# Performance work log

Measured on AMD Instinct MI355X. Metric: run time of the kernel, lower is better.

## Reference

```python
import jax, jax.numpy as jnp
import numpy as np

N_AGENTS = 10
N_ENEMIES = 11
N_ALLIES = 9
H = 64           # rnn_hidden_dim
HYP = 64         # api_hyper_dim
DEPTH = 2        # residual_depth
OWN = 32
EF = 10          # enemy_feats_dim
AF = 10          # ally_feats_dim
N_ACTIONS = 17
BS = 1024


def _hypernet(x, win, bin_, wres, bres, wout, bout):
    # Linear -> ReLU -> DEPTH x (ReLU(Linear)+identity) -> Linear
    h = jax.nn.relu(x @ win + bin_)
    for d in range(DEPTH):
        h = jax.nn.relu(h @ wres[d] + bres[d]) + h
    return h @ wout + bout


def _gru_cell(x, h, wi, wh, bi, bh):
    gi = x @ wi + bi
    gh = h @ wh + bh
    ir, iz, in_ = jnp.split(gi, 3, axis=-1)
    hr, hz, hn = jnp.split(gh, 3, axis=-1)
    r = jax.nn.sigmoid(ir + hr)
    z = jax.nn.sigmoid(iz + hz)
    n = jnp.tanh(in_ + r * hn)
    return (1.0 - z) * n + z * h


def setup_inputs() -> dict:
    key = jax.random.key(0)
    ks = iter(jax.random.split(key, 48))
    def p(shape, s=0.1):
        return jax.random.normal(next(ks), shape, jnp.float32) * s
    N = BS * N_AGENTS
    inp = {
        'own_feats':    p((N, OWN), 1.0),
        'enemy_feats':  p((N * N_ENEMIES, EF), 1.0),
        'ally_feats':   p((N * N_ALLIES, AF), 1.0),
        'hidden_state': p((N, H), 1.0),
        'fc1_w': p((OWN, H)), 'fc1_b': p((H,)),
        'agent_emb': p((N_AGENTS, H)), 'action_emb': p((N_ACTIONS, H)),
        'hen_win': p((EF, HYP)), 'hen_bin': p((HYP,)),
        'hen_wres': p((DEPTH, HYP, HYP)), 'hen_bres': p((DEPTH, HYP)),
        'hen_wout': p((HYP, EF * H)), 'hen_bout': p((EF * H,)),
        'hal_win': p((AF, HYP)), 'hal_bin': p((HYP,)),
        'hal_wres': p((DEPTH, HYP, HYP)), 'hal_bres': p((DEPTH, HYP)),
        'hal_wout': p((HYP, AF * H)), 'hal_bout': p((AF * H,)),
        'gru_wi': p((H, 3 * H)), 'gru_wh': p((H, 3 * H)),
        'gru_bi': p((3 * H,)), 'gru_bh': p((3 * H,)),
        'fc2_w': p((H, 6)), 'fc2_b': p((6,)),
        'how_win': p((EF, HYP)), 'how_bin': p((HYP,)),
        'how_wres': p((DEPTH, HYP, HYP)), 'how_bres': p((DEPTH, HYP)),
        'how_wout': p((HYP, H)), 'how_bout': p((H,)),
        'hob_win': p((EF, HYP)), 'hob_bin': p((HYP,)),
        'hob_wres': p((DEPTH, HYP, HYP)), 'hob_bres': p((DEPTH, HYP)),
        'hob_wout': p((HYP, 1)), 'hob_bout': p((1,)),
        'agent_idx': jax.random.randint(next(ks), (N,), 0, N_AGENTS),
        'last_action_idx': jax.random.randint(next(ks), (N,), 0, N_ACTIONS),
        'bs': BS,
    }
    return inp


def reference(own_feats, enemy_feats, ally_feats, hidden_state,
              fc1_w, fc1_b, agent_emb, action_emb,
              hen_win, hen_bin, hen_wres, hen_bres, hen_wout, hen_bout,
              hal_win, hal_bin, hal_wres, hal_bres, hal_wout, hal_bout,
              gru_wi, gru_wh, gru_bi, gru_bh,
              fc2_w, fc2_b,
              how_win, how_bin, how_wres, how_bres, how_wout, how_bout,
              hob_win, hob_bin, hob_wres, hob_bres, hob_wout, hob_bout,
              agent_idx, last_action_idx, bs):
    N = bs * N_AGENTS
    # own embedding + id embeddings
    emb = own_feats @ fc1_w + fc1_b
    emb = emb + agent_emb[agent_idx] + action_emb[last_action_idx]
    # per-enemy hypernet weights [N*NE, EF, H]; bmm + sum-pool over enemies
    w_en = _hypernet(enemy_feats, hen_win, hen_bin, hen_wres, hen_bres,
                     hen_wout, hen_bout).reshape(-1, EF, H)
    emb_en = jnp.einsum('nf,nfh->nh', enemy_feats, w_en)
    emb_en = emb_en.reshape(N, N_ENEMIES, H).sum(axis=1)
    # per-ally hypernet weights + bmm + sum-pool
    w_al = _hypernet(ally_feats, hal_win, hal_bin, hal_wres, hal_bres,
                     hal_wout, hal_bout).reshape(-1, AF, H)
    emb_al = jnp.einsum('nf,nfh->nh', ally_feats, w_al)
    emb_al = emb_al.reshape(N, N_ALLIES, H).sum(axis=1)
    x = jax.nn.relu(emb + emb_en + emb_al)
    hh = _gru_cell(x, hidden_state.reshape(-1, H), gru_wi, gru_wh, gru_bi, gru_bh)
    q_normal = (hh @ fc2_w + fc2_b).reshape(bs, N_AGENTS, 6)
    # attack-action head: hypernet-generated per-enemy weights/biases
    ow = _hypernet(enemy_feats, how_win, how_bin, how_wres, how_bres,
                   how_wout, how_bout).reshape(N, N_ENEMIES, H)
    ob = _hypernet(enemy_feats, hob_win, hob_bin, hob_wres, hob_bres,
                   hob_wout, hob_bout).reshape(N, N_ENEMIES)
    q_attack = (jnp.einsum('nh,neh->ne', hh, ow) + ob).reshape(bs, N_AGENTS, N_ENEMIES)
    q = jnp.concatenate([q_normal, q_attack], axis=-1)
    return q, hh.reshape(bs, N_AGENTS, H)
```

## Files before the change

### kernel.cpp

```cpp
#include <hip/hip_runtime.h>

#define DI static __device__ __forceinline__

typedef short s16x8 __attribute__((ext_vector_type(8)));
typedef float f32x4 __attribute__((ext_vector_type(4)));
typedef float f32x2 __attribute__((ext_vector_type(2)));
typedef unsigned u32x2 __attribute__((ext_vector_type(2)));

DI unsigned short f2b(float f) {
  union { float f; unsigned u; } v; v.f = f;
  return (unsigned short)((v.u + 0x7FFF + ((v.u >> 16) & 1)) >> 16);
}
DI float b2f(unsigned short s) {
  union { unsigned u; float f; } v; v.u = ((unsigned)s) << 16;
  return v.f;
}
DI unsigned cvtpk(float lo, float hi) {
  unsigned r;
  asm("v_cvt_pk_bf16_f32 %0, %1, %2" : "=v"(r) : "v"(lo), "v"(hi));
  return r;
}
DI f32x4 MFMA(s16x8 a, s16x8 b, f32x4 c) {
  return __builtin_amdgcn_mfma_f32_16x16x32_bf16(a, b, c, 0, 0, 0);
}
DI s16x8 ldg8(const unsigned short* p) { return *(const s16x8*)p; }

#define OFF_WEN   0
#define OFF_WAL   10240
#define OFF_WHOW  20480
#define OFF_WHOB  30720
#define OFF_BGEN  40960
#define OFF_BGAL  83968
#define OFF_WIT   126976
#define OFF_WHT   139264
#define OFF_FC1T  151552
#define OFF_FC2E  153600
#define OFF_HOWT  154624
#define OFF_HOBT  158720
#define SH_END    159744
#define B_EMB_EN  (SH_END*2)
#define B_EMB_AL  (B_EMB_EN + 2621440)
#define B_HB      (B_EMB_AL + 2621440)
#define B_GBF     (B_HB + 40960)

#define XSTR 40
#define HSTR 72
#define PSTR 680

__global__ __launch_bounds__(256) void kprep(
    const float* __restrict__ hen_win, const float* __restrict__ hen_wres,
    const float* __restrict__ hal_win, const float* __restrict__ hal_wres,
    const float* __restrict__ how_win, const float* __restrict__ how_wres,
    const float* __restrict__ hob_win, const float* __restrict__ hob_wres,
    const float* __restrict__ hen_wout, const float* __restrict__ hen_bout,
    const float* __restrict__ hal_wout, const float* __restrict__ hal_bout,
    const float* __restrict__ gru_wi, const float* __restrict__ gru_wh,
    const float* __restrict__ fc1_w, const float* __restrict__ fc2_w,
    const float* __restrict__ how_bout, const float* __restrict__ how_wout,
    const float* __restrict__ hob_wout,
    unsigned short* __restrict__ ws)
{
  const int gid = blockIdx.x * 256 + threadIdx.x;
  const int gsz = gridDim.x * 256;
  for (int i = gid; i < 4 * 10240; i += gsz) {
    int s = i / 10240, idx = i - s * 10240;
    const float* win  = (s == 0) ? hen_win  : (s == 1) ? hal_win  : (s == 2) ? how_win  : hob_win;
    const float* wres = (s == 0) ? hen_wres : (s == 1) ? hal_wres : (s == 2) ? how_wres : hob_wres;
    float v;
    if (idx < 2048) { int n = idx >> 5, k = idx & 31; v = (k < 10) ? win[k*64 + n] : 0.f; }
    else { int r = idx - 2048; int d = r >> 12; int r2 = r & 4095; int n = r2 >> 6, k = r2 & 63;
           v = wres[d*4096 + k*64 + n]; }
    ws[s * 10240 + idx] = f2b(v);
  }
  for (int i = gid; i < 2 * 43008; i += gsz) {
    int s = i / 43008, idx = i - s * 43008;
    const float* wout = s ? hal_wout : hen_wout;
    const float* bout = s ? hal_bout : hen_bout;
    int kl = idx & 31, n = (idx >> 5) & 63, c = idx >> 11;
    int kfg = c * 32 + kl;
    float v = 0.f;
    if (kfg < 640)      { int k = kfg / 10, f = kfg - k * 10; v = wout[k*640 + f*64 + n]; }
    else if (kfg < 650) { v = bout[(kfg - 640)*64 + n]; }
    ws[(s ? OFF_BGAL : OFF_BGEN) + idx] = f2b(v);
  }
  for (int i = gid; i < 2 * 12288; i += gsz) {
    int s = i / 12288, idx = i - s * 12288;
    int n = idx >> 6, k = idx & 63;
    const float* w = s ? gru_wh : gru_wi;
    ws[(s ? OFF_WHT : OFF_WIT) + idx] = f2b(w[k*192 + n]);
  }
  for (int i = gid; i < 2048; i += gsz) { int n = i >> 5, k = i & 31; ws[OFF_FC1T + i] = f2b(fc1_w[k*64 + n]); }
  for (int i = gid; i < 1024; i += gsz) {
    int n = i >> 6, k = i & 63;
    float v = 0.f; if (n < 6) v = fc2_w[k*6 + n]; else if (n == 6) v = how_bout[k];
    ws[OFF_FC2E + i] = f2b(v);
  }
  for (int i = gid; i < 4096; i += gsz) ws[OFF_HOWT + i] = f2b(how_wout[i]);
}

template<int TMAX, bool WLAST>
DI void stack_batch(const unsigned short* __restrict__ x_lds,
                    unsigned short* const (&hbp)[TMAX], const int (&tis)[TMAX], int E,
                    const unsigned short* __restrict__ wg,
                    const float* __restrict__ bin, const float* __restrict__ bres,
                    f32x4 (&hval)[TMAX][4])
{
  const int l = threadIdx.x & 63;
  const int lrow = l & 15, gq = l >> 4, lk8 = gq * 8;
  {
    s16x8 wf[4]; f32x4 bv[4];
#pragma unroll
    for (int mt = 0; mt < 4; mt++) {
      wf[mt] = ldg8(wg + (mt*16 + lrow)*32 + lk8);
      bv[mt] = *(const f32x4*)(bin + mt*16 + gq*4);
    }
#pragma unroll
    for (int tt = 0; tt < TMAX; tt++) {
      if (tis[tt] < E) {
        s16x8 xf = *(const s16x8*)&x_lds[(tis[tt]*16 + lrow)*XSTR + lk8];
#pragma unroll
        for (int mt = 0; mt < 4; mt++) {
          f32x4 d = MFMA(wf[mt], xf, f32x4{0.f,0.f,0.f,0.f});
#pragma unroll
          for (int r = 0; r < 4; r++) hval[tt][mt][r] = fmaxf(d[r] + bv[mt][r], 0.f);
        }
        unsigned short* wr = hbp[tt] + lrow*HSTR;
#pragma unroll
        for (int mt = 0; mt < 4; mt++) {
          u32x2 pw;
          pw.x = cvtpk(hval[tt][mt][0], hval[tt][mt][1]);
          pw.y = cvtpk(hval[tt][mt][2], hval[tt][mt][3]);
          *(u32x2*)&wr[mt*16 + gq*4] = pw;
        }
      }
    }
  }
#pragma unroll
  for (int d = 0; d < 2; d++) {
    const unsigned short* wt = wg + 2048 + d * 4096;
    s16x8 wf[4][2]; f32x4 bv[4];
#pragma unroll
    for (int mt = 0; mt < 4; mt++) {
      wf[mt][0] = ldg8(wt + (mt*16 + lrow)*64 + lk8);
      wf[mt][1] = ldg8(wt + (mt*16 + lrow)*64 + 32 + lk8);
      bv[mt] = *(const f32x4*)(bres + d*64 + mt*16 + gq*4);
    }
#pragma unroll
    for (int tt = 0; tt < TMAX; tt++) {
      if (tis[tt] < E) {
        const unsigned short* hr = hbp[tt] + lrow*HSTR;
        s16x8 b0 = *(const s16x8*)&hr[lk8];
        s16x8 b1 = *(const s16x8*)&hr[32 + lk8];
#pragma unroll
        for (int mt = 0; mt < 4; mt++) {
          f32x4 a = MFMA(wf[mt][0], b0, f32x4{0.f,0.f,0.f,0.f});
          a = MFMA(wf[mt][1], b1, a);
#pragma unroll
          for (int r = 0; r < 4; r++)
            hval[tt][mt][r] = fmaxf(a[r] + bv[mt][r], 0.f) + hval[tt][mt][r];
        }
        if (d == 0 || WLAST) {
          unsigned short* wr = hbp[tt] + lrow*HSTR;
#pragma unroll
          for (int mt = 0; mt < 4; mt++) {
            u32x2 pw;
            pw.x = cvtpk(hval[tt][mt][0], hval[tt][mt][1]);
            pw.y = cvtpk(hval[tt][mt][2], hval[tt][mt][3]);
            *(u32x2*)&wr[mt*16 + gq*4] = pw;
          }
        }
      }
    }
  }
}

template<int E>
DI void hyp_body16(const float* __restrict__ feats,
                   const unsigned short* __restrict__ Wg, const unsigned short* __restrict__ Bg,
                   const float* __restrict__ bin, const float* __restrict__ bres,
                   float* __restrict__ emb, char* smem)
{
  unsigned short* x_lds = (unsigned short*)smem;
  unsigned short* h_lds = (unsigned short*)(smem + 14080);
  unsigned short* P     = (unsigned short*)smem;
  const int t = threadIdx.x;
  const int l = t & 63, wv = t >> 6;
  const int lrow = l & 15, gq = l >> 4, lk8 = gq * 8, lr4 = gq * 4;

  for (int idx = t; idx < E * 512; idx += 256) {
    int row = idx >> 5, c = idx & 31;
    x_lds[row*XSTR + c] = (c < 10) ? f2b(feats[row*10 + c]) : (unsigned short)0;
  }
  __syncthreads();

  int tis[3] = {wv, wv + 4, wv + 8};
  unsigned short* hbp[3] = { h_lds + (wv)*16*HSTR, h_lds + (wv+4)*16*HSTR, h_lds + (wv+8)*16*HSTR };
  f32x4 hval[3][4];
  stack_batch<3, true>(x_lds, hbp, tis, E, Wg, bin, bres, hval);
  __syncthreads();

  const int a = t >> 4, kq = t & 15, k0 = kq * 4;
  float acc[4][10];
#pragma unroll
  for (int kk = 0; kk < 4; kk++)
#pragma unroll
    for (int f = 0; f < 10; f++) acc[kk][f] = 0.f;
#pragma unroll
  for (int e = 0; e < E; e++) {
    int row = a * E + e;
    const unsigned short* xr = x_lds + row * XSTR;
    s16x8 xv8 = *(const s16x8*)xr;
    unsigned xv2 = *(const unsigned*)(xr + 8);
    float xf[10];
#pragma unroll
    for (int f = 0; f < 8; f++) xf[f] = b2f((unsigned short)xv8[f]);
    xf[8] = b2f((unsigned short)(xv2 & 0xFFFF));
    xf[9] = b2f((unsigned short)(xv2 >> 16));
    u32x2 hp = *(const u32x2*)&h_lds[row*HSTR + k0];
    float hf[4] = { b2f((unsigned short)(hp.x & 0xFFFF)), b2f((unsigned short)(hp.x >> 16)),
                    b2f((unsigned short)(hp.y & 0xFFFF)), b2f((unsigned short)(hp.y >> 16)) };
#pragma unroll
    for (int kk = 0; kk < 4; kk++)
#pragma unroll
      for (int f = 0; f < 10; f++) acc[kk][f] += hf[kk] * xf[f];
  }
  float sxv = 0.f; int a2 = 0, fx = 0;
  if (t < 160) {
    a2 = t / 10; fx = t - a2 * 10;
    for (int e = 0; e < E; e++) sxv += feats[(a2*E + e)*10 + fx];
  }
  __syncthreads();

  u32x2* Pw = (u32x2*)(P + a*PSTR + k0*10);
#pragma unroll
  for (int m = 0; m < 10; m++) {
    const int s0 = 4*m, s1 = 4*m+1, s2 = 4*m+2, s3 = 4*m+3;
    u32x2 pw;
    pw.x = cvtpk(acc[s0/10][s0%10], acc[s1/10][s1%10]);
    pw.y = cvtpk(acc[s2/10][s2%10], acc[s3/10][s3%10]);
    Pw[m] = pw;
  }
  if (t < 160) P[a2*PSTR + 640 + fx] = f2b(sxv);
  for (int i = t; i < 352; i += 256) { int a3 = i / 22, c = i - a3*22; P[a3*PSTR + 650 + c] = 0; }
  __syncthreads();

  f32x4 acc0 = {0.f,0.f,0.f,0.f}, acc1 = {0.f,0.f,0.f,0.f};
  const unsigned short* Bw = Bg + (wv*16 + lrow)*32 + lk8;
#pragma unroll
  for (int c = 0; c < 21; c++) {
    s16x8 af = *(const s16x8*)&P[lrow*PSTR + c*32 + lk8];
    s16x8 bf = ldg8(Bw + c*2048);
    if (c & 1) acc1 = MFMA(af, bf, acc1); else acc0 = MFMA(af, bf, acc0);
  }
#pragma unroll
  for (int r = 0; r < 4; r++)
    emb[(lr4 + r)*64 + wv*16 + lrow] = acc0[r] + acc1[r];
}

__global__ __launch_bounds__(256) void khyp_ea(
    const float* __restrict__ en_feats, const float* __restrict__ al_feats,
    const unsigned short* __restrict__ ws,
    const float* __restrict__ en_bin, const float* __restrict__ en_bres,
    const float* __restrict__ al_bin, const float* __restrict__ al_bres,
    float* __restrict__ emb_en, float* __restrict__ emb_al)
{
  __shared__ __align__(16) char smem[39424];
  if (blockIdx.x < 640) {
    int blk = blockIdx.x;
    hyp_body16<11>(en_feats + (long)blk*1760, ws + OFF_WEN, ws + OFF_BGEN,
                   en_bin, en_bres, emb_en + (long)blk*1024, smem);
  } else {
    int blk = blockIdx.x - 640;
    hyp_body16<9>(al_feats + (long)blk*1440, ws + OFF_WAL, ws + OFF_BGAL,
                  al_bin, al_bres, emb_al + (long)blk*1024, smem);
  }
}

__global__ __launch_bounds__(256) void kfused(
    const float* __restrict__ own, const float* __restrict__ agent_emb,
    const float* __restrict__ action_emb,
    const int* __restrict__ agent_idx, const int* __restrict__ last_action,
    const float* __restrict__ emb_en, const float* __restrict__ emb_al,
    const float* __restrict__ hidden,
    const unsigned short* __restrict__ ws,
    const float* __restrict__ fc1_b, const float* __restrict__ bi,
    const float* __restrict__ bh, const float* __restrict__ fc2_b,
    float* __restrict__ qout, float* __restrict__ hhout,
    unsigned short* __restrict__ g_bf, float* __restrict__ hb)
{
  __shared__ unsigned short own_lds[16*32];
  __shared__ unsigned short x_lds[16*HSTR];
  __shared__ unsigned short hp_lds[16*HSTR];
  __shared__ unsigned short hh_lds[16*HSTR];
  const int t = threadIdx.x;
  const int l = t & 63, wv = t >> 6;
  const int lrow = l & 15, lk8 = (l >> 4) * 8, lr4 = (l >> 4) * 4;
  const int n0 = blockIdx.x * 16;

  const unsigned short* fc1T = ws + OFF_FC1T;
  const unsigned short* wiT  = ws + OFF_WIT;
  const unsigned short* whT  = ws + OFF_WHT;
  const unsigned short* howT = ws + OFF_HOWT;
  const unsigned short* fc2e = ws + OFF_FC2E;

  for (int i = t; i < 512; i += 256) own_lds[i] = f2b(own[n0*32 + i]);
  for (int i = t; i < 1024; i += 256) hp_lds[(i >> 6)*HSTR + (i & 63)] = f2b(hidden[n0*64 + i]);
  __syncthreads();

  const int j = wv * 16 + lrow;
  {
    s16x8 a0 = *(const s16x8*)&own_lds[lrow*32 + lk8];
    s16x8 b0 = ldg8(fc1T + (wv*16 + lrow)*32 + lk8);
    f32x4 c0 = MFMA(a0, b0, f32x4{0.f,0.f,0.f,0.f});
    float fb = fc1_b[j];
#pragma unroll
    for (int r = 0; r < 4; r++) {
      int aa = lr4 + r; int n = n0 + aa;
      int ai = agent_idx[n], la = last_action[n];
      float v = c0[r] + fb + agent_emb[ai*64 + j] + action_emb[la*64 + j]
              + emb_en[n*64 + j] + emb_al[n*64 + j];
      x_lds[aa*HSTR + j] = f2b(fmaxf(v, 0.f));
    }
  }
  __syncthreads();

  {
    s16x8 xa[2], ha[2];
#pragma unroll
    for (int s = 0; s < 2; s++) {
      xa[s] = *(const s16x8*)&x_lds[lrow*HSTR + s*32 + lk8];
      ha[s] = *(const s16x8*)&hp_lds[lrow*HSTR + s*32 + lk8];
    }
    f32x4 gi[3], gh[3];
#pragma unroll
    for (int g3 = 0; g3 < 3; g3++) { gi[g3] = f32x4{0.f,0.f,0.f,0.f}; gh[g3] = f32x4{0.f,0.f,0.f,0.f}; }
#pragma unroll
    for (int g3 = 0; g3 < 3; g3++) {
      int tl = wv + g3 * 4;
#pragma unroll
      for (int s = 0; s < 2; s++) {
        gi[g3] = MFMA(xa[s], ldg8(wiT + (tl*16 + lrow)*64 + s*32 + lk8), gi[g3]);
        gh[g3] = MFMA(ha[s], ldg8(whT + (tl*16 + lrow)*64 + s*32 + lk8), gh[g3]);
      }
    }
    float bir = bi[j], biz = bi[64 + j], bin_ = bi[128 + j];
    float bhr = bh[j], bhz = bh[64 + j], bhn = bh[128 + j];
#pragma unroll
    for (int r = 0; r < 4; r++) {
      int aa = lr4 + r; int n = n0 + aa;
      float rr = 1.f / (1.f + __expf(-(gi[0][r] + bir + gh[0][r] + bhr)));
      float zz = 1.f / (1.f + __expf(-(gi[1][r] + biz + gh[1][r] + bhz)));
      float nn = tanhf(gi[2][r] + bin_ + rr * (gh[2][r] + bhn));
      float hp = hidden[n*64 + j];
      float hhv = (1.f - zz) * nn + zz * hp;
      hhout[n*64 + j] = hhv;
      hh_lds[aa*HSTR + j] = f2b(hhv);
    }
  }
  __syncthreads();

  {
    s16x8 hha[2];
#pragma unroll
    for (int s = 0; s < 2; s++) hha[s] = *(const s16x8*)&hh_lds[lrow*HSTR + s*32 + lk8];
    f32x4 gc = {0.f,0.f,0.f,0.f};
#pragma unroll
    for (int s = 0; s < 2; s++) gc = MFMA(hha[s], ldg8(howT + (wv*16 + lrow)*64 + s*32 + lk8), gc);
#pragma unroll
    for (int r = 0; r < 4; r++) g_bf[(n0 + lr4 + r)*64 + wv*16 + lrow] = f2b(gc[r]);
    if (wv == 0) {
      f32x4 qc = {0.f,0.f,0.f,0.f};
#pragma unroll
      for (int s = 0; s < 2; s++) qc = MFMA(hha[s], ldg8(fc2e + lrow*64 + s*32 + lk8), qc);
#pragma unroll
      for (int r = 0; r < 4; r++) {
        int n = n0 + lr4 + r;
        if (lrow < 6)       qout[n*17 + lrow] = qc[r] + fc2_b[lrow];
        else if (lrow == 6) hb[n] = qc[r];
      }
    }
  }
}

__global__ __launch_bounds__(256) void kattack(
    const float* __restrict__ en_feats, const unsigned short* __restrict__ ws,
    const float* __restrict__ how_bin, const float* __restrict__ how_bres,
    const float* __restrict__ hob_bin, const float* __restrict__ hob_bres,
    const unsigned short* __restrict__ g_bf, const float* __restrict__ hbuf,
    const float* __restrict__ hob_wout, const float* __restrict__ hob_bout,
    float* __restrict__ qout)
{
  __shared__ __align__(16) char smem[41728];
  unsigned short* x_lds = (unsigned short*)smem;
  unsigned short* scr   = (unsigned short*)(smem + 14080);
  const int t = threadIdx.x;
  const int l = t & 63, wv = t >> 6;
  const int lrow = l & 15, gq = l >> 4;
  const int blk = blockIdx.x;
  const float* feats = en_feats + (long)blk * 1760;

  for (int idx = t; idx < 176*32; idx += 256) {
    int row = idx >> 5, c = idx & 31;
    x_lds[row*XSTR + c] = (c < 10) ? f2b(feats[row*10 + c]) : (unsigned short)0;
  }
  __syncthreads();

  int tis[3] = {wv, wv + 4, wv + 8};
  unsigned short* hbp[3] = { scr + (wv*3+0)*16*HSTR, scr + (wv*3+1)*16*HSTR, scr + (wv*3+2)*16*HSTR };
  f32x4 hval[3][4];

  stack_batch<3, false>(x_lds, hbp, tis, 11, ws + OFF_WHOB, hob_bin, hob_bres, hval);
  f32x4 hw[4];
#pragma unroll
  for (int mt = 0; mt < 4; mt++) hw[mt] = *(const f32x4*)(hob_wout + mt*16 + gq*4);
  float qbv[3] = {0.f, 0.f, 0.f};
#pragma unroll
  for (int tt = 0; tt < 3; tt++) {
    if (tis[tt] < 11) {
      float s = 0.f;
#pragma unroll
      for (int mt = 0; mt < 4; mt++)
#pragma unroll
        for (int r = 0; r < 4; r++) s += hval[tt][mt][r] * hw[mt][r];
      s += __shfl_xor(s, 16, 64);
      s += __shfl_xor(s, 32, 64);
      qbv[tt] = s;
    }
  }

  stack_batch<3, false>(x_lds, hbp, tis, 11, ws + OFF_WHOW, how_bin, how_bres, hval);
  const float hob_b0 = hob_bout[0];
#pragma unroll
  for (int tt = 0; tt < 3; tt++) {
    if (tis[tt] < 11) {
      int row = tis[tt]*16 + lrow;
      int ag = (unsigned)row / 11u;
      int n = blk*16 + ag;
      float s = 0.f;
#pragma unroll
      for (int mt = 0; mt < 4; mt++) {
        u32x2 gv = *(const u32x2*)(g_bf + (long)n*64 + mt*16 + gq*4);
        s += hval[tt][mt][0] * b2f((unsigned short)(gv.x & 0xFFFF))
           + hval[tt][mt][1] * b2f((unsigned short)(gv.x >> 16))
           + hval[tt][mt][2] * b2f((unsigned short)(gv.y & 0xFFFF))
           + hval[tt][mt][3] * b2f((unsigned short)(gv.y >> 16));
      }
      s += __shfl_xor(s, 16, 64);
      s += __shfl_xor(s, 32, 64);
      if (l < 16) {
        int e = row - ag * 11;
        qout[n*17 + 6 + e] = s + qbv[tt] + hbuf[n] + hob_b0;
      }
    }
  }
}

extern "C" void kernel_launch(void* const* d_in, const int* in_sizes, int n_in,
                              void* d_out, int out_size, void* d_ws, size_t ws_size,
                              hipStream_t stream)
{
  (void)in_sizes; (void)n_in; (void)out_size; (void)ws_size;
  const float* own        = (const float*)d_in[0];
  const float* enemy      = (const float*)d_in[1];
  const float* ally       = (const float*)d_in[2];
  const float* hidden     = (const float*)d_in[3];
  const float* fc1_w      = (const float*)d_in[4];
  const float* fc1_b      = (const float*)d_in[5];
  const float* agent_emb  = (const float*)d_in[6];
  const float* action_emb = (const float*)d_in[7];
  const float* hen_win  = (const float*)d_in[8];  const float* hen_bin  = (const float*)d_in[9];
  const float* hen_wres = (const float*)d_in[10]; const float* hen_bres = (const float*)d_in[11];
  const float* hen_wout = (const float*)d_in[12]; const float* hen_bout = (const float*)d_in[13];
  const float* hal_win  = (const float*)d_in[14]; const float* hal_bin  = (const float*)d_in[15];
  const float* hal_wres = (const float*)d_in[16]; const float* hal_bres = (const float*)d_in[17];
  const float* hal_wout = (const float*)d_in[18]; const float* hal_bout = (const float*)d_in[19];
  const float* gru_wi = (const float*)d_in[20];   const float* gru_wh = (const float*)d_in[21];
  const float* gru_bi = (const float*)d_in[22];   const float* gru_bh = (const float*)d_in[23];
  const float* fc2_w  = (const float*)d_in[24];   const float* fc2_b  = (const float*)d_in[25];
  const float* how_win  = (const float*)d_in[26]; const float* how_bin  = (const float*)d_in[27];
  const float* how_wres = (const float*)d_in[28]; const float* how_bres = (const float*)d_in[29];
  const float* how_wout = (const float*)d_in[30]; const float* how_bout = (const float*)d_in[31];
  const float* hob_win  = (const float*)d_in[32]; const float* hob_bin  = (const float*)d_in[33];
  const float* hob_wres = (const float*)d_in[34]; const float* hob_bres = (const float*)d_in[35];
  const float* hob_wout = (const float*)d_in[36]; const float* hob_bout = (const float*)d_in[37];
  const int* agent_idx   = (const int*)d_in[38];
  const int* last_action = (const int*)d_in[39];

  unsigned short* ws = (unsigned short*)d_ws;
  float* emb_en = (float*)((char*)d_ws + B_EMB_EN);
  float* emb_al = (float*)((char*)d_ws + B_EMB_AL);
  float* hb     = (float*)((char*)d_ws + B_HB);
  unsigned short* g_bf = (unsigned short*)((char*)d_ws + B_GBF);

  float* q  = (float*)d_out;
  float* hh = q + 1024*10*17;

  kprep<<<128, 256, 0, stream>>>(hen_win, hen_wres, hal_win, hal_wres,
      how_win, how_wres, hob_win, hob_wres,
      hen_wout, hen_bout, hal_wout, hal_bout,
      gru_wi, gru_wh, fc1_w, fc2_w, how_bout, how_wout, hob_wout, ws);
  khyp_ea<<<1280, 256, 0, stream>>>(enemy, ally, ws,
      hen_bin, hen_bres, hal_bin, hal_bres, emb_en, emb_al);
  kfused<<<640, 256, 0, stream>>>(own, agent_emb, action_emb, agent_idx, last_action,
      emb_en, emb_al, hidden, ws, fc1_b, gru_bi, gru_bh, fc2_b, q, hh, g_bf, hb);
  kattack<<<640, 256, 0, stream>>>(enemy, ws, how_bin, how_bres, hob_bin, hob_bres,
      g_bf, hb, hob_wout, hob_bout, q);
}
```

Before: 78.49 us.

## Make hypernet embedding kernel persistent with double-buffered feature staging and swizzled LDS

New measurement: 78.05 us. No clear change (-0.6%).

```diff
diff --git a/kernel.cpp b/kernel.cpp
--- a/kernel.cpp
+++ b/kernel.cpp
@@ -4,7 +4,6 @@
 
 typedef short s16x8 __attribute__((ext_vector_type(8)));
 typedef float f32x4 __attribute__((ext_vector_type(4)));
-typedef float f32x2 __attribute__((ext_vector_type(2)));
 typedef unsigned u32x2 __attribute__((ext_vector_type(2)));
 
 DI unsigned short f2b(float f) {
@@ -36,16 +35,20 @@
 #define OFF_FC1T  151552
 #define OFF_FC2E  153600
 #define OFF_HOWT  154624
-#define OFF_HOBT  158720
 #define SH_END    159744
 #define B_EMB_EN  (SH_END*2)
 #define B_EMB_AL  (B_EMB_EN + 2621440)
 #define B_HB      (B_EMB_AL + 2621440)
 #define B_GBF     (B_HB + 40960)
 
+#define PSTR 680
+#define HSTR 72
 #define XSTR 40
-#define HSTR 72
-#define PSTR 680
+
+#define SLOT 28160
+#define XBC  5632
+DI int xoffc(int row, int b) { return ((row*32  + b) ^ ((row & 7) << 4)); }
+DI int hoffc(int row, int b) { return XBC + ((row*128 + b) ^ ((row & 7) << 4)); }
 
 __global__ __launch_bounds__(256) void kprep(
     const float* __restrict__ hen_win, const float* __restrict__ hen_wres,
@@ -57,7 +60,6 @@
     const float* __restrict__ gru_wi, const float* __restrict__ gru_wh,
     const float* __restrict__ fc1_w, const float* __restrict__ fc2_w,
     const float* __restrict__ how_bout, const float* __restrict__ how_wout,
-    const float* __restrict__ hob_wout,
     unsigned short* __restrict__ ws)
 {
   const int gid = blockIdx.x * 256 + threadIdx.x;
@@ -98,15 +100,21 @@
   for (int i = gid; i < 4096; i += gsz) ws[OFF_HOWT + i] = f2b(how_wout[i]);
 }
 
-template<int TMAX, bool WLAST>
-DI void stack_batch(const unsigned short* __restrict__ x_lds,
-                    unsigned short* const (&hbp)[TMAX], const int (&tis)[TMAX], int E,
-                    const unsigned short* __restrict__ wg,
-                    const float* __restrict__ bin, const float* __restrict__ bres,
-                    f32x4 (&hval)[TMAX][4])
-{
-  const int l = threadIdx.x & 63;
+DI void stage_item(const float* __restrict__ feats, int vrows, char* sl) {
+  for (int idx = threadIdx.x; idx < 176*16; idx += 256) {
+    int row = idx >> 4, c = idx & 15;
+    float v = (row < vrows && c < 10) ? feats[row*10 + c] : 0.f;
+    *(unsigned short*)(sl + xoffc(row, c*2)) = f2b(v);
+  }
+}
+
+DI void stackP(char* sl, int ntiles, const unsigned short* __restrict__ wg,
+               const float* __restrict__ bin, const float* __restrict__ bres)
+{
+  const int l = threadIdx.x & 63, wv = threadIdx.x >> 6;
   const int lrow = l & 15, gq = l >> 4, lk8 = gq * 8;
+  const int tis[3] = {wv, wv + 4, wv + 8};
+  f32x4 hval[3][4];
   {
     s16x8 wf[4]; f32x4 bv[4];
 #pragma unroll
@@ -115,22 +123,18 @@
       bv[mt] = *(const f32x4*)(bin + mt*16 + gq*4);
     }
 #pragma unroll
-    for (int tt = 0; tt < TMAX; tt++) {
-      if (tis[tt] < E) {
-        s16x8 xf = *(const s16x8*)&x_lds[(tis[tt]*16 + lrow)*XSTR + lk8];
+    for (int tt = 0; tt < 3; tt++) {
+      if (tis[tt] < ntiles) {
+        int row = tis[tt]*16 + lrow;
+        s16x8 xf = *(const s16x8*)(sl + xoffc(row, gq*16));
 #pragma unroll
         for (int mt = 0; mt < 4; mt++) {
-          f32x4 d = MFMA(wf[mt], xf, f32x4{0.f,0.f,0.f,0.f});
-#pragma unroll
-          for (int r = 0; r < 4; r++) hval[tt][mt][r] = fmaxf(d[r] + bv[mt][r], 0.f);
-        }
-        unsigned short* wr = hbp[tt] + lrow*HSTR;
-#pragma unroll
-        for (int mt = 0; mt < 4; mt++) {
-          u32x2 pw;
-          pw.x = cvtpk(hval[tt][mt][0], hval[tt][mt][1]);
+          f32x4 d = MFMA(wf[mt], xf, bv[mt]);
+#pragma unroll
+          for (int r = 0; r < 4; r++) hval[tt][mt][r] = fmaxf(d[r], 0.f);
+          u32x2 pw; pw.x = cvtpk(hval[tt][mt][0], hval[tt][mt][1]);
           pw.y = cvtpk(hval[tt][mt][2], hval[tt][mt][3]);
-          *(u32x2*)&wr[mt*16 + gq*4] = pw;
+          *(u32x2*)(sl + hoffc(row, (mt*16 + gq*4)*2)) = pw;
         }
       }
     }
@@ -138,123 +142,33 @@
 #pragma unroll
   for (int d = 0; d < 2; d++) {
     const unsigned short* wt = wg + 2048 + d * 4096;
-    s16x8 wf[4][2]; f32x4 bv[4];
+    s16x8 wf0[4], wf1[4]; f32x4 bv[4];
 #pragma unroll
     for (int mt = 0; mt < 4; mt++) {
-      wf[mt][0] = ldg8(wt + (mt*16 + lrow)*64 + lk8);
-      wf[mt][1] = ldg8(wt + (mt*16 + lrow)*64 + 32 + lk8);
+      wf0[mt] = ldg8(wt + (mt*16 + lrow)*64 + lk8);
+      wf1[mt] = ldg8(wt + (mt*16 + lrow)*64 + 32 + lk8);
       bv[mt] = *(const f32x4*)(bres + d*64 + mt*16 + gq*4);
     }
 #pragma unroll
-    for (int tt = 0; tt < TMAX; tt++) {
-      if (tis[tt] < E) {
-        const unsigned short* hr = hbp[tt] + lrow*HSTR;
-        s16x8 b0 = *(const s16x8*)&hr[lk8];
-        s16x8 b1 = *(const s16x8*)&hr[32 + lk8];
+    for (int tt = 0; tt < 3; tt++) {
+      if (tis[tt] < ntiles) {
+        int row = tis[tt]*16 + lrow;
+        s16x8 b0 = *(const s16x8*)(sl + hoffc(row, gq*16));
+        s16x8 b1 = *(const s16x8*)(sl + hoffc(row, 64 + gq*16));
 #pragma unroll
         for (int mt = 0; mt < 4; mt++) {
-          f32x4 a = MFMA(wf[mt][0], b0, f32x4{0.f,0.f,0.f,0.f});
-          a = MFMA(wf[mt][1], b1, a);
+          f32x4 acc = MFMA(wf0[mt], b0, bv[mt]);
+          acc = MFMA(wf1[mt], b1, acc);
 #pragma unroll
           for (int r = 0; r < 4; r++)
-            hval[tt][mt][r] = fmaxf(a[r] + bv[mt][r], 0.f) + hval[tt][mt][r];
+            hval[tt][mt][r] = fmaxf(acc[r], 0.f) + hval[tt][mt][r];
+          u32x2 pw; pw.x = cvtpk(hval[tt][mt][0], hval[tt][mt][1]);
+          pw.y = cvtpk(hval[tt][mt][2], hval[tt][mt][3]);
+          *(u32x2*)(sl + hoffc(row, (mt*16 + gq*4)*2)) = pw;
         }
-        if (d == 0 || WLAST) {
-          unsigned short* wr = hbp[tt] + lrow*HSTR;
-#pragma unroll
-          for (int mt = 0; mt < 4; mt++) {
-            u32x2 pw;
-            pw.x = cvtpk(hval[tt][mt][0], hval[tt][mt][1]);
-            pw.y = cvtpk(hval[tt][mt][2], hval[tt][mt][3]);
-            *(u32x2*)&wr[mt*16 + gq*4] = pw;
-          }
-        }
-      }
-    }
-  }
-}
-
-template<int E>
-DI void hyp_body16(const float* __restrict__ feats,
-                   const unsigned short* __restrict__ Wg, const unsigned short* __restrict__ Bg,
-                   const float* __restrict__ bin, const float* __restrict__ bres,
-                   float* __restrict__ emb, char* smem)
-{
-  unsigned short* x_lds = (unsigned short*)smem;
-  unsigned short* h_lds = (unsigned short*)(smem + 14080);
-  unsigned short* P     = (unsigned short*)smem;
-  const int t = threadIdx.x;
-  const int l = t & 63, wv = t >> 6;
-  const int lrow = l & 15, gq = l >> 4, lk8 = gq * 8, lr4 = gq * 4;
-
-  for (int idx = t; idx < E * 512; idx += 256) {
-    int row = idx >> 5, c = idx & 31;
-    x_lds[row*XSTR + c] = (c < 10) ? f2b(feats[row*10 + c]) : (unsigned short)0;
-  }
-  __syncthreads();
-
-  int tis[3] = {wv, wv + 4, wv + 8};
-  unsigned short* hbp[3] = { h_lds + (wv)*16*HSTR, h_lds + (wv+4)*16*HSTR, h_lds + (wv+8)*16*HSTR };
-  f32x4 hval[3][4];
-  stack_batch<3, true>(x_lds, hbp, tis, E, Wg, bin, bres, hval);
-  __syncthreads();
-
-  const int a = t >> 4, kq = t & 15, k0 = kq * 4;
-  float acc[4][10];
-#pragma unroll
-  for (int kk = 0; kk < 4; kk++)
-#pragma unroll
-    for (int f = 0; f < 10; f++) acc[kk][f] = 0.f;
-#pragma unroll
-  for (int e = 0; e < E; e++) {
-    int row = a * E + e;
-    const unsigned short* xr = x_lds + row * XSTR;
-    s16x8 xv8 = *(const s16x8*)xr;
-    unsigned xv2 = *(const unsigned*)(xr + 8);
-    float xf[10];
-#pragma unroll
-    for (int f = 0; f < 8; f++) xf[f] = b2f((unsigned short)xv8[f]);
-    xf[8] = b2f((unsigned short)(xv2 & 0xFFFF));
-    xf[9] = b2f((unsigned short)(xv2 >> 16));
-    u32x2 hp = *(const u32x2*)&h_lds[row*HSTR + k0];
-    float hf[4] = { b2f((unsigned short)(hp.x & 0xFFFF)), b2f((unsigned short)(hp.x >> 16)),
-                    b2f((unsigned short)(hp.y & 0xFFFF)), b2f((unsigned short)(hp.y >> 16)) };
-#pragma unroll
-    for (int kk = 0; kk < 4; kk++)
-#pragma unroll
-      for (int f = 0; f < 10; f++) acc[kk][f] += hf[kk] * xf[f];
-  }
-  float sxv = 0.f; int a2 = 0, fx = 0;
-  if (t < 160) {
-    a2 = t / 10; fx = t - a2 * 10;
-    for (int e = 0; e < E; e++) sxv += feats[(a2*E + e)*10 + fx];
-  }
-  __syncthreads();
-
-  u32x2* Pw = (u32x2*)(P + a*PSTR + k0*10);
-#pragma unroll
-  for (int m = 0; m < 10; m++) {
-    const int s0 = 4*m, s1 = 4*m+1, s2 = 4*m+2, s3 = 4*m+3;
-    u32x2 pw;
-    pw.x = cvtpk(acc[s0/10][s0%10], acc[s1/10][s1%10]);
-    pw.y = cvtpk(acc[s2/10][s2%10], acc[s3/10][s3%10]);
-    Pw[m] = pw;
-  }
-  if (t < 160) P[a2*PSTR + 640 + fx] = f2b(sxv);
-  for (int i = t; i < 352; i += 256) { int a3 = i / 22, c = i - a3*22; P[a3*PSTR + 650 + c] = 0; }
-  __syncthreads();
-
-  f32x4 acc0 = {0.f,0.f,0.f,0.f}, acc1 = {0.f,0.f,0.f,0.f};
-  const unsigned short* Bw = Bg + (wv*16 + lrow)*32 + lk8;
-#pragma unroll
-  for (int c = 0; c < 21; c++) {
-    s16x8 af = *(const s16x8*)&P[lrow*PSTR + c*32 + lk8];
-    s16x8 bf = ldg8(Bw + c*2048);
-    if (c & 1) acc1 = MFMA(af, bf, acc1); else acc0 = MFMA(af, bf, acc0);
-  }
-#pragma unroll
-  for (int r = 0; r < 4; r++)
-    emb[(lr4 + r)*64 + wv*16 + lrow] = acc0[r] + acc1[r];
+      }
+    }
+  }
 }
 
 __global__ __launch_bounds__(256) void khyp_ea(
@@ -264,15 +178,97 @@
     const float* __restrict__ al_bin, const float* __restrict__ al_bres,
     float* __restrict__ emb_en, float* __restrict__ emb_al)
 {
-  __shared__ __align__(16) char smem[39424];
-  if (blockIdx.x < 640) {
-    int blk = blockIdx.x;
-    hyp_body16<11>(en_feats + (long)blk*1760, ws + OFF_WEN, ws + OFF_BGEN,
-                   en_bin, en_bres, emb_en + (long)blk*1024, smem);
-  } else {
-    int blk = blockIdx.x - 640;
-    hyp_body16<9>(al_feats + (long)blk*1440, ws + OFF_WAL, ws + OFF_BGAL,
-                  al_bin, al_bres, emb_al + (long)blk*1024, smem);
+  __shared__ __align__(16) char smem[2*SLOT];
+  const int t = threadIdx.x;
+  const int l = t & 63, wv = t >> 6;
+  const int lrow = l & 15, gq = l >> 4, lk8 = gq * 8;
+
+  int its[3]; int nit = 0;
+  for (int it = blockIdx.x; it < 1280; it += 512) its[nit++] = it;
+
+  {
+    int it0 = its[0];
+    const float* f0 = (it0 < 640) ? en_feats + (long)it0*1760
+                                  : al_feats + (long)(it0-640)*1440;
+    stage_item(f0, (it0 < 640) ? 176 : 144, smem);
+  }
+  __syncthreads();
+
+  for (int i = 0; i < nit; i++) {
+    char* sl = smem + (i & 1) * SLOT;
+    const int it = its[i];
+    const bool en = it < 640;
+    const int E = en ? 11 : 9;
+    const float* feats = en ? en_feats + (long)it*1760 : al_feats + (long)(it-640)*1440;
+    const unsigned short* Wg = ws + (en ? OFF_WEN : OFF_WAL);
+    const unsigned short* Bg = ws + (en ? OFF_BGEN : OFF_BGAL);
+    const float* bin  = en ? en_bin  : al_bin;
+    const float* bres = en ? en_bres : al_bres;
+    float* emb = en ? emb_en + (long)it*1024 : emb_al + (long)(it-640)*1024;
+
+    stackP(sl, E, Wg, bin, bres);
+    __syncthreads();
+
+    const int a = t >> 4, kq = t & 15, k0 = kq * 4;
+    float acc[4][10];
+#pragma unroll
+    for (int kk = 0; kk < 4; kk++)
+#pragma unroll
+      for (int f = 0; f < 10; f++) acc[kk][f] = 0.f;
+    for (int e = 0; e < E; e++) {
+      int row = a * E + e;
+      s16x8 xv8 = *(const s16x8*)(sl + xoffc(row, 0));
+      unsigned xv2 = *(const unsigned*)(sl + xoffc(row, 16));
+      float xf[10];
+#pragma unroll
+      for (int f = 0; f < 8; f++) xf[f] = b2f((unsigned short)xv8[f]);
+      xf[8] = b2f((unsigned short)(xv2 & 0xFFFF));
+      xf[9] = b2f((unsigned short)(xv2 >> 16));
+      u32x2 hp = *(const u32x2*)(sl + hoffc(row, k0*2));
+      float hf[4] = { b2f((unsigned short)(hp.x & 0xFFFF)), b2f((unsigned short)(hp.x >> 16)),
+                      b2f((unsigned short)(hp.y & 0xFFFF)), b2f((unsigned short)(hp.y >> 16)) };
+#pragma unroll
+      for (int kk = 0; kk < 4; kk++)
+#pragma unroll
+        for (int f = 0; f < 10; f++) acc[kk][f] += hf[kk] * xf[f];
+    }
+    float sxv = 0.f; int a2 = 0, fx = 0;
+    if (t < 160) {
+      a2 = t / 10; fx = t - a2 * 10;
+      for (int e = 0; e < E; e++) sxv += feats[(a2*E + e)*10 + fx];
+    }
+    __syncthreads();
+
+    unsigned short* P2 = (unsigned short*)sl;
+    {
+      unsigned* Pw = (unsigned*)(P2 + a*PSTR + k0*10);
+#pragma unroll
+      for (int m = 0; m < 20; m++) {
+        const int v0 = 2*m, v1 = 2*m + 1;
+        Pw[m] = cvtpk(acc[v0/10][v0%10], acc[v1/10][v1%10]);
+      }
+    }
+    if (t < 160) P2[a2*PSTR + 640 + fx] = f2b(sxv);
+    if (t < 352) { int a3 = t / 22, c = t - a3*22; P2[a3*PSTR + 650 + c] = 0; }
+    if (i + 1 < nit) {
+      int itn = its[i+1];
+      const float* fn = (itn < 640) ? en_feats + (long)itn*1760
+                                    : al_feats + (long)(itn-640)*1440;
+      stage_item(fn, (itn < 640) ? 176 : 144, smem + ((i+1) & 1) * SLOT);
+    }
+    __syncthreads();
+
+    f32x4 g0 = {0.f,0.f,0.f,0.f}, g1 = {0.f,0.f,0.f,0.f};
+    const unsigned short* Bw = Bg + (wv*16 + lrow)*32 + lk8;
+#pragma unroll
+    for (int c = 0; c < 21; c++) {
+      s16x8 af = *(const s16x8*)&P2[lrow*PSTR + c*32 + lk8];
+      s16x8 bf = ldg8(Bw + c*2048);
+      if (c & 1) g1 = MFMA(af, bf, g1); else g0 = MFMA(af, bf, g0);
+    }
+#pragma unroll
+    for (int r = 0; r < 4; r++)
+      emb[(gq*4 + r)*64 + wv*16 + lrow] = g0[r] + g1[r];
   }
 }
 
@@ -318,7 +314,7 @@
       int aa = lr4 + r; int n = n0 + aa;
       int ai = agent_idx[n], la = last_action[n];
       float v = c0[r] + fb + agent_emb[ai*64 + j] + action_emb[la*64 + j]
-              + emb_en[n*64 + j] + emb_al[n*64 + j];
+              + emb_en[(long)n*64 + j] + emb_al[(long)n*64 + j];
       x_lds[aa*HSTR + j] = f2b(fmaxf(v, 0.f));
     }
   }
@@ -382,6 +378,82 @@
   }
 }
 
+template<int TMAX, bool WLAST>
+DI void stack_batch(const unsigned short* __restrict__ x_lds,
+                    unsigned short* const (&hbp)[TMAX], const int (&tis)[TMAX], int NT,
+                    const unsigned short* __restrict__ wg,
+                    const float* __restrict__ bin, const float* __restrict__ bres,
+                    f32x4 (&hval)[TMAX][4])
+{
+  const int l = threadIdx.x & 63;
+  const int lrow = l & 15, gq = l >> 4, lk8 = gq * 8;
+  {
+    s16x8 wf[4]; f32x4 bv[4];
+#pragma unroll
+    for (int mt = 0; mt < 4; mt++) {
+      wf[mt] = ldg8(wg + (mt*16 + lrow)*32 + lk8);
+      bv[mt] = *(const f32x4*)(bin + mt*16 + gq*4);
+    }
+#pragma unroll
+    for (int tt = 0; tt < TMAX; tt++) {
+      if (tis[tt] < NT) {
+        s16x8 xf = *(const s16x8*)&x_lds[(tis[tt]*16 + lrow)*XSTR + lk8];
+#pragma unroll
+        for (int mt = 0; mt < 4; mt++) {
+          f32x4 d = MFMA(wf[mt], xf, bv[mt]);
+#pragma unroll
+          for (int r = 0; r < 4; r++) hval[tt][mt][r] = fmaxf(d[r], 0.f);
+        }
+        unsigned short* wr = hbp[tt] + lrow*HSTR;
+#pragma unroll
+        for (int mt = 0; mt < 4; mt++) {
+          u32x2 pw;
+          pw.x = cvtpk(hval[tt][mt][0], hval[tt][mt][1]);
+          pw.y = cvtpk(hval[tt][mt][2], hval[tt][mt][3]);
+          *(u32x2*)&wr[mt*16 + gq*4] = pw;
+        }
+      }
+    }
+  }
+#pragma unroll
+  for (int d = 0; d < 2; d++) {
+    const unsigned short* wt = wg + 2048 + d * 4096;
+    s16x8 wf[4][2]; f32x4 bv[4];
+#pragma unroll
+    for (int mt = 0; mt < 4; mt++) {
+      wf[mt][0] = ldg8(wt + (mt*16 + lrow)*64 + lk8);
+      wf[mt][1] = ldg8(wt + (mt*16 + lrow)*64 + 32 + lk8);
+      bv[mt] = *(const f32x4*)(bres + d*64 + mt*16 + gq*4);
+    }
+#pragma unroll
+    for (int tt = 0; tt < TMAX; tt++) {
+      if (tis[tt] < NT) {
+        const unsigned short* hr = hbp[tt] + lrow*HSTR;
+        s16x8 b0 = *(const s16x8*)&hr[lk8];
+        s16x8 b1 = *(const s16x8*)&hr[32 + lk8];
+#pragma unroll
+        for (int mt = 0; mt < 4; mt++) {
+          f32x4 a = MFMA(wf[mt][0], b0, bv[mt]);
+          a = MFMA(wf[mt][1], b1, a);
+#pragma unroll
+          for (int r = 0; r < 4; r++)
+            hval[tt][mt][r] = fmaxf(a[r], 0.f) + hval[tt][mt][r];
+        }
+        if (d == 0 || WLAST) {
+          unsigned short* wr = hbp[tt] + lrow*HSTR;
+#pragma unroll
+          for (int mt = 0; mt < 4; mt++) {
+            u32x2 pw;
+            pw.x = cvtpk(hval[tt][mt][0], hval[tt][mt][1]);
+            pw.y = cvtpk(hval[tt][mt][2], hval[tt][mt][3]);
+            *(u32x2*)&wr[mt*16 + gq*4] = pw;
+          }
+        }
+      }
+    }
+  }
+}
+
 __global__ __launch_bounds__(256) void kattack(
     const float* __restrict__ en_feats, const unsigned short* __restrict__ ws,
     const float* __restrict__ how_bin, const float* __restrict__ how_bres,
@@ -434,8 +506,8 @@
   for (int tt = 0; tt < 3; tt++) {
     if (tis[tt] < 11) {
       int row = tis[tt]*16 + lrow;
-      int ag = (unsigned)row / 11u;
-      int n = blk*16 + ag;
+      unsigned ag = (unsigned)row / 11u;
+      int n = blk*16 + (int)ag;
       float s = 0.f;
 #pragma unroll
       for (int mt = 0; mt < 4; mt++) {
@@ -448,7 +520,7 @@
       s += __shfl_xor(s, 16, 64);
       s += __shfl_xor(s, 32, 64);
       if (l < 16) {
-        int e = row - ag * 11;
+        int e = row - (int)ag * 11;
         qout[n*17 + 6 + e] = s + qbv[tt] + hbuf[n] + hob_b0;
       }
     }
@@ -498,8 +570,8 @@
   kprep<<<128, 256, 0, stream>>>(hen_win, hen_wres, hal_win, hal_wres,
       how_win, how_wres, hob_win, hob_wres,
       hen_wout, hen_bout, hal_wout, hal_bout,
-      gru_wi, gru_wh, fc1_w, fc2_w, how_bout, how_wout, hob_wout, ws);
-  khyp_ea<<<1280, 256, 0, stream>>>(enemy, ally, ws,
+      gru_wi, gru_wh, fc1_w, fc2_w, how_bout, how_wout, ws);
+  khyp_ea<<<512, 256, 0, stream>>>(enemy, ally, ws,
       hen_bin, hen_bres, hal_bin, hal_bres, emb_en, emb_al);
   kfused<<<640, 256, 0, stream>>>(own, agent_emb, action_emb, agent_idx, last_action,
       emb_en, emb_al, hidden, ws, fc1_b, gru_bi, gru_bh, fc2_b, q, hh, g_bf, hb);
```
